# Kernel tuning notes

Hardware: AMD Instinct MI355X
Metric: run time of the kernel (lower is better)

The kernel has to match this reference:

```python
import jax, jax.numpy as jnp
import numpy as np

MUL = 128
LS = (0, 1, 2, 3, 4)
LMAX = 4
DIM = MUL * sum(2 * l + 1 for l in LS)   # 3200
NUM_IRREPS = MUL * len(LS)               # 640
NUM_M = [MUL * (LMAX + 1 - m) for m in range(LMAX + 1)]
N = 16384


def _expm(A, order=24, squarings=10):
    A = A / (2.0 ** squarings)
    E = np.eye(A.shape[0])
    T = np.eye(A.shape[0])
    for k in range(1, order):
        T = T @ A / k
        E = E + T
    for _ in range(squarings):
        E = E @ E
    return E


def _su2_generators(j):
    m = np.arange(-j, j)
    raising = np.diag(-np.sqrt(j * (j + 1) - m * (m + 1)), k=-1).astype(complex)
    m = np.arange(-j + 1, j + 1)
    lowering = np.diag(np.sqrt(j * (j + 1) - m * (m - 1)), k=1).astype(complex)
    m = np.arange(-j, j + 1)
    return np.stack([0.5 * (raising + lowering), np.diag(1j * m), -0.5j * (raising - lowering)])


def _q_real_to_complex(l):
    q = np.zeros((2 * l + 1, 2 * l + 1), dtype=complex)
    for m in range(-l, 0):
        q[l + m, l + abs(m)] = 1 / np.sqrt(2)
        q[l + m, l - abs(m)] = -1j / np.sqrt(2)
    q[l, l] = 1.0
    for m in range(1, l + 1):
        q[l + m, l + abs(m)] = (-1) ** m / np.sqrt(2)
        q[l + m, l - abs(m)] = 1j * (-1) ** m / np.sqrt(2)
    return (-1j) ** l * q


def _so3_generators(l):
    X = _su2_generators(l)
    Q = _q_real_to_complex(l)
    return np.real(np.conj(Q.T)[None] @ X @ Q[None])


def _J(l):
    # J_l = pi rotation about (x+y)/sqrt(2): conjugates z_rot (y-axis) into the beta (x-axis) rotation,
    # reproducing e3nn's _Jd used in wigner_D = Z(a) J Z(b) J Z(g).
    X = _so3_generators(l)
    return _expm(np.pi * (X[0] + X[1]) / np.sqrt(2.0))


JMAT = {l: jnp.asarray(_J(l), dtype=jnp.float32) for l in LS if l > 0}


def _build_mask():
    mask = np.zeros((LMAX + 1, DIM), dtype=bool)
    cur = 0
    for l in LS:
        for k in range(MUL):
            base = cur + k * (2 * l + 1)
            for m in range(l + 1):
                if m == 0:
                    mask[0, base + l] = True
                else:
                    mask[m, base + l + m] = True
                    mask[m, base + l - m] = True
        cur += MUL * (2 * l + 1)
    return mask


_MASK = _build_mask()
IDX = [np.nonzero(_MASK[m])[0] for m in range(LMAX + 1)]  # same layout for in and out irreps


def _z_rot(angle, l):
    d = 2 * l + 1
    freqs = jnp.arange(l, -l - 1, -1, dtype=angle.dtype)
    c = jnp.cos(freqs * angle[:, None])
    s = jnp.sin(freqs * angle[:, None])
    i = jnp.arange(d)
    M = jnp.zeros((angle.shape[0], d, d), angle.dtype)
    M = M.at[:, i, i].set(c)
    M = M.at[:, i, d - 1 - i].add(s)
    return M


def _wigner(l, alpha, beta, gamma):
    J = JMAT[l].astype(alpha.dtype)
    return _z_rot(alpha, l) @ J @ _z_rot(beta, l) @ J @ _z_rot(gamma, l)


def _forward(x, R, fc0_w, fc0_b, w_ms):
    n = x.shape[0]
    # xyz_to_angles(R[:, [1, 2, 0]])
    v = jnp.stack([R[:, 1], R[:, 2], R[:, 0]], axis=-1)
    v = v / jnp.clip(jnp.linalg.norm(v, axis=-1, keepdims=True), 1e-12)
    v = jnp.clip(v, -1.0, 1.0)
    beta = jnp.arccos(v[:, 1])
    alpha = jnp.arctan2(v[:, 0], v[:, 2])
    gamma = jnp.zeros_like(alpha)
    rots = {l: _wigner(l, alpha, beta, gamma) for l in LS if l > 0}
    # rotate input blocks; the l=0 block of x_rot stays zero (exactly as the torch source)
    parts = []
    off = 0
    for l in LS:
        d = 2 * l + 1
        size = MUL * d
        if l == 0:
            parts.append(jnp.zeros((n, size), x.dtype))
        else:
            blk = x[:, off:off + size].reshape(n, MUL, d)
            parts.append(jnp.einsum('nji,nmj->nmi', rots[l], blk).reshape(n, size))
        off += size
    x_rot = jnp.concatenate(parts, axis=1)
    out = jnp.zeros((n, DIM), x.dtype)
    # m = 0 path (radial_emb=False => w = ones, a no-op multiply)
    out = out.at[:, IDX[0]].add(x_rot[:, IDX[0]] @ fc0_w.T + fc0_b)
    # m >= 1 SO(2) paths
    for m in range(1, LMAX + 1):
        co = NUM_M[m]
        seg = x_rot[:, IDX[m]].reshape(n, 2, co)
        y = jnp.einsum('nct,ot->nco', seg, w_ms[m - 1])  # (n, 2, 2*co)
        re = y[:, 0, :co] - y[:, 1, co:]
        im = y[:, 0, co:] + y[:, 1, :co]
        out = out.at[:, IDX[m]].add(jnp.stack((re, im), axis=1).reshape(n, -1))
    # rotate output blocks (l=0 untouched)
    parts = []
    off = 0
    for l in LS:
        d = 2 * l + 1
        size = MUL * d
        blk = out[:, off:off + size]
        if l > 0:
            blk = jnp.einsum('nji,nmj->nmi', rots[l], blk.reshape(n, MUL, d)).reshape(n, size)
        parts.append(blk)
        off += size
    return jnp.concatenate(parts, axis=1)


def setup_inputs() -> dict:
    key = jax.random.key(0)
    ks = jax.random.split(key, 8)
    x = jax.random.normal(ks[0], (N, DIM), jnp.float32)
    R = jax.random.normal(ks[1], (N, 3), jnp.float32)
    fc0_w = jax.random.normal(ks[2], (NUM_IRREPS, NUM_IRREPS), jnp.float32) / np.float32(np.sqrt(NUM_IRREPS))
    fc0_b = jnp.zeros((NUM_IRREPS,), jnp.float32)
    w1 = jax.random.normal(ks[3], (2 * NUM_M[1], NUM_M[1]), jnp.float32) / np.float32(np.sqrt(2.0 * NUM_M[1]))
    w2 = jax.random.normal(ks[4], (2 * NUM_M[2], NUM_M[2]), jnp.float32) / np.float32(np.sqrt(2.0 * NUM_M[2]))
    w3 = jax.random.normal(ks[5], (2 * NUM_M[3], NUM_M[3]), jnp.float32) / np.float32(np.sqrt(2.0 * NUM_M[3]))
    w4 = jax.random.normal(ks[6], (2 * NUM_M[4], NUM_M[4]), jnp.float32) / np.float32(np.sqrt(2.0 * NUM_M[4]))
    return {"x": x, "R": R, "fc0_w": fc0_w, "fc0_b": fc0_b, "w1": w1, "w2": w2, "w3": w3, "w4": w4}


def reference(x, R, fc0_w, fc0_b, w1, w2, w3, w4):
    return _forward(x, R, fc0_w, fc0_b, (w1, w2, w3, w4))
```

## Files before the change

### kernel.cpp

```cpp
#include <hip/hip_runtime.h>
#include <hip/hip_bf16.h>
#include <math.h>

#define N_ROWS 16384
#define DIM    3200

using short8  = __attribute__((ext_vector_type(8))) short;
using floatx4 = __attribute__((ext_vector_type(4))) float;

__device__ const int c_K [5] = {640, 1024, 768, 512, 256};
__device__ const int c_UO[5] = {0, 640, 1664, 2432, 2944};
__device__ const int c_WO[5] = {0, 409600, 1458176, 2048000, 2310144};
__device__ const int c_mOf[25]  = {0,0,0,0,0, 1,1,1,1,1,1,1,1, 2,2,2,2,2,2, 3,3,3,3, 4,4};
__device__ const int c_ntOf[25] = {0,1,2,3,4, 0,1,2,3,4,5,6,7, 0,1,2,3,4,5, 0,1,2,3, 0,1};

__device__ __forceinline__ constexpr int joff_of(int l) { return l==1 ? 0 : l==2 ? 9 : l==3 ? 34 : 83; }
__device__ __forceinline__ constexpr int gO(int m)      { return m==1 ? 640 : m==2 ? 1664 : m==3 ? 2432 : 2944; }

__global__ __launch_bounds__(128) void build_J(float* __restrict__ Jout)
{
    const int l = blockIdx.x + 1;
    const int d = 2*l + 1;
    const int dd = d*d;
    const int tid = threadIdx.x;
    __shared__ double Qr[81], Qi[81], Xr[81], Xi[81];
    __shared__ double M1r[81], M1i[81];
    __shared__ double Am[81], Em[81], Tm[81], Tn[81];

    if (tid == 0) {
        for (int e = 0; e < dd; ++e) { Qr[e]=0; Qi[e]=0; Xr[e]=0; Xi[e]=0; }
        const double jj = (double)l;
        for (int i = 0; i < d-1; ++i) {
            double mm = -jj + (double)i;
            Xr[(i+1)*d + i] += 0.5 * (-sqrt(jj*(jj+1.0) - mm*(mm+1.0)));
            double m2 = -jj + 1.0 + (double)i;
            Xr[i*d + (i+1)] += 0.5 * ( sqrt(jj*(jj+1.0) - m2*(m2-1.0)));
        }
        for (int i = 0; i < d; ++i) Xi[i*d + i] = -jj + (double)i;
        const double is2 = 1.0 / sqrt(2.0);
        for (int mm = -l; mm < 0; ++mm) {
            int r = l + mm;
            Qr[r*d + (l - mm)] = is2;
            Qi[r*d + (l + mm)] = -is2;
        }
        Qr[l*d + l] = 1.0;
        for (int mm = 1; mm <= l; ++mm) {
            int r = l + mm;
            double sgn = (mm & 1) ? -1.0 : 1.0;
            Qr[r*d + (l + mm)] = sgn * is2;
            Qi[r*d + (l - mm)] = sgn * is2;
        }
        double fr, fi;
        switch (l & 3) {
            case 0: fr = 1;  fi = 0;  break;
            case 1: fr = 0;  fi = -1; break;
            case 2: fr = -1; fi = 0;  break;
            default: fr = 0; fi = 1;  break;
        }
        for (int e = 0; e < dd; ++e) {
            double qr = Qr[e], qi = Qi[e];
            Qr[e] = qr*fr - qi*fi;
            Qi[e] = qr*fi + qi*fr;
        }
    }
    __syncthreads();
    const int i = tid / d;
    const int j = tid % d;
    if (tid < dd) {
        double ar = 0, ai = 0;
        for (int k = 0; k < d; ++k) {
            double xr = Xr[i*d+k], xi = Xi[i*d+k];
            double qr = Qr[k*d+j], qi = Qi[k*d+j];
            ar += xr*qr - xi*qi;
            ai += xr*qi + xi*qr;
        }
        M1r[tid] = ar; M1i[tid] = ai;
    }
    __syncthreads();
    if (tid < dd) {
        double ar = 0;
        for (int k = 0; k < d; ++k)
            ar += Qr[k*d+i]*M1r[k*d+j] + Qi[k*d+i]*M1i[k*d+j];
        const double scale = 3.14159265358979323846 / sqrt(2.0) / 1024.0;
        Am[tid] = ar * scale;
        Em[tid] = (i == j) ? 1.0 : 0.0;
        Tm[tid] = (i == j) ? 1.0 : 0.0;
    }
    __syncthreads();
    for (int k = 1; k < 24; ++k) {
        if (tid < dd) {
            double s = 0;
            for (int b = 0; b < d; ++b) s += Tm[i*d+b] * Am[b*d+j];
            Tn[tid] = s / (double)k;
        }
        __syncthreads();
        if (tid < dd) { Tm[tid] = Tn[tid]; Em[tid] += Tn[tid]; }
        __syncthreads();
    }
    for (int s = 0; s < 10; ++s) {
        if (tid < dd) {
            double v = 0;
            for (int b = 0; b < d; ++b) v += Em[i*d+b] * Em[b*d+j];
            Tn[tid] = v;
        }
        __syncthreads();
        if (tid < dd) Em[tid] = Tn[tid];
        __syncthreads();
    }
    if (tid < dd) Jout[joff_of(l) + tid] = (float)Em[tid];
}

__global__ __launch_bounds__(256) void prep_w(
    const float* __restrict__ fc0_w,
    const float* __restrict__ w1, const float* __restrict__ w2,
    const float* __restrict__ w3, const float* __restrict__ w4,
    __hip_bfloat16* __restrict__ Wall)
{
    const int m = blockIdx.y;
    const int idx = blockIdx.x * 256 + threadIdx.x;
    if (m == 0) {
        if (idx < 640*640) Wall[idx] = __float2bfloat16(fc0_w[idx]);
        return;
    }
    const int co = 128 * (5 - m);
    const int C  = 2 * co;
    if (idx >= C*C) return;
    const float* wm = (m==1) ? w1 : (m==2) ? w2 : (m==3) ? w3 : w4;
    const int jj = idx / C;
    const int tt = idx - jj * C;
    float v;
    if (jj < co) {
        v = (tt < co) ? wm[jj*co + tt] : -wm[(co + jj)*co + (tt - co)];
    } else {
        v = (tt < co) ? wm[jj*co + tt] :  wm[(jj - co)*co + (tt - co)];
    }
    Wall[c_WO[m] + idx] = __float2bfloat16(v);
}

__global__ __launch_bounds__(256) void build_trig(
    const float* __restrict__ R, float* __restrict__ trig)
{
    const int row = blockIdx.x * 256 + threadIdx.x;
    if (row >= N_ROWS) return;
    float r0 = R[row*3+0], r1 = R[row*3+1], r2 = R[row*3+2];
    float nrm = sqrtf(r0*r0 + r1*r1 + r2*r2);
    nrm = fmaxf(nrm, 1e-12f);
    float vx = r1/nrm, vy = r2/nrm, vz = r0/nrm;
    vx = fminf(1.f, fmaxf(-1.f, vx));
    vy = fminf(1.f, fmaxf(-1.f, vy));
    vz = fminf(1.f, fmaxf(-1.f, vz));
    float beta  = acosf(vy);
    float alpha = atan2f(vx, vz);
    float* t = trig + row*20;
#pragma unroll
    for (int m = 0; m < 5; ++m) {
        float s, c;
        sincosf(alpha * (float)m, &s, &c);
        t[m] = c; t[5+m] = s;
        sincosf(beta * (float)m, &s, &c);
        t[10+m] = c; t[15+m] = s;
    }
}

__global__ __launch_bounds__(256) void build_D(
    const float* __restrict__ Jws, const float* __restrict__ trig,
    float* __restrict__ Dws)
{
    const int gid = blockIdx.x * 256 + threadIdx.x;
    if (gid >= N_ROWS * 164) return;
    const int row = gid / 164;
    const int e   = gid - row * 164;
    int l, base;
    if (e < 9)       { l = 1; base = 0;  }
    else if (e < 34) { l = 2; base = 9;  }
    else if (e < 83) { l = 3; base = 34; }
    else             { l = 4; base = 83; }
    const int d = 2*l + 1;
    const int loc = e - base;
    const int i = loc / d, j = loc - i*d;
    const float* Jp = Jws + base;
    const float* t  = trig + row*20;
    float pij = 0.f, pdj = 0.f;
    for (int b = 0; b < d; ++b) {
        int f = l - b; int af = f < 0 ? -f : f;
        float cb = t[10 + af];
        float sb = (b >= l) ? t[15 + b - l] : -t[15 + l - b];
        float zr  = Jp[i*d + b]*cb + Jp[i*d + (d-1-b)]*sb;
        float zr2 = Jp[(d-1-i)*d + b]*cb + Jp[(d-1-i)*d + (d-1-b)]*sb;
        float jb  = Jp[b*d + j];
        pij += zr  * jb;
        pdj += zr2 * jb;
    }
    int f = l - i; int af = f < 0 ? -f : f;
    float ca = t[af];
    float sa = (f > 0) ? t[5 + f] : ((f < 0) ? -t[5 + af] : 0.f);
    Dws[gid] = ca * pij + sa * pdj;
}

template<int L>
__device__ __forceinline__ void rot_one(const float* __restrict__ xr,
                                        const float* __restrict__ Dl,
                                        __hip_bfloat16* __restrict__ Urow, int k)
{
    constexpr int d = 2*L + 1;
    float xv[d], y[d];
    const float* xp = xr + 128*L*L + k*d;
#pragma unroll
    for (int j = 0; j < d; ++j) xv[j] = xp[j];
#pragma unroll
    for (int q = 0; q < d; ++q) {
        float acc = 0.f;
#pragma unroll
        for (int j = 0; j < d; ++j) acc += Dl[j*d + q] * xv[j];
        y[q] = acc;
    }
    Urow[L*128 + k] = __float2bfloat16(y[L]);
#pragma unroll
    for (int m = 1; m <= L; ++m) {
        unsigned short lo = __builtin_bit_cast(unsigned short, __float2bfloat16(y[L-m]));
        unsigned short hi = __builtin_bit_cast(unsigned short, __float2bfloat16(y[L+m]));
        unsigned int pack = ((unsigned int)hi << 16) | lo;
        *(unsigned int*)(Urow + gO(m) + 2*((L-m)*128 + k)) = pack;
    }
}

template<int L>
__device__ __forceinline__ void unrot_one(const __hip_bfloat16* __restrict__ Yrow,
                                          const float* __restrict__ Dl,
                                          float* __restrict__ orow, int k)
{
    constexpr int d = 2*L + 1;
    float yv[d];
    yv[L] = __bfloat162float(Yrow[L*128 + k]);
#pragma unroll
    for (int m = 1; m <= L; ++m) {
        unsigned int pack = *(const unsigned int*)(Yrow + gO(m) + 2*((L-m)*128 + k));
        unsigned short lo = (unsigned short)(pack & 0xffffu);
        unsigned short hi = (unsigned short)(pack >> 16);
        yv[L-m] = __bfloat162float(__builtin_bit_cast(__hip_bfloat16, lo));
        yv[L+m] = __bfloat162float(__builtin_bit_cast(__hip_bfloat16, hi));
    }
    float* op = orow + 128*L*L + k*d;
#pragma unroll
    for (int i = 0; i < d; ++i) {
        float acc = 0.f;
#pragma unroll
        for (int j = 0; j < d; ++j) acc += Dl[j*d + i] * yv[j];
        op[i] = acc;
    }
}

__global__ __launch_bounds__(256) void rot_gather(
    const float* __restrict__ x, const float* __restrict__ Dws,
    __hip_bfloat16* __restrict__ U)
{
    const int gid = blockIdx.x * 256 + threadIdx.x;
    const int row = gid / 640;
    const int c   = gid - row * 640;
    const int l = c >> 7, k = c & 127;
    const float* xr = x + (size_t)row * DIM;
    __hip_bfloat16* Urow = U + (size_t)row * DIM;
    const float* Dm = Dws + (size_t)row * 164;
    switch (l) {
        case 0: Urow[k] = __float2bfloat16(0.f); break;
        case 1: rot_one<1>(xr, Dm + 0,  Urow, k); break;
        case 2: rot_one<2>(xr, Dm + 9,  Urow, k); break;
        case 3: rot_one<3>(xr, Dm + 34, Urow, k); break;
        case 4: rot_one<4>(xr, Dm + 83, Urow, k); break;
    }
}

__device__ __forceinline__ void g2lds16(const void* g, void* l) {
    __builtin_amdgcn_global_load_lds(
        (const __attribute__((address_space(1))) void*)g,
        (__attribute__((address_space(3))) void*)l, 16, 0, 0);
}

__global__ __launch_bounds__(256) void gemm_bt(
    const __hip_bfloat16* __restrict__ U, const __hip_bfloat16* __restrict__ W,
    const float* __restrict__ bias, __hip_bfloat16* __restrict__ Y)
{
    const int by = blockIdx.y;
    const int m  = c_mOf[by];
    const int nt = c_ntOf[by];
    const int K  = c_K[m];
    const int row0 = blockIdx.x * 128;
    const __hip_bfloat16* Ablk = U + (size_t)row0*DIM + c_UO[m];
    const __hip_bfloat16* Bblk = W + c_WO[m] + (size_t)nt*128*K;
    __shared__ __align__(16) __hip_bfloat16 As[128*32];
    __shared__ __align__(16) __hip_bfloat16 Bs[128*32];
    const int tid  = threadIdx.x;
    const int lane = tid & 63, w = tid >> 6;
    const int frow = lane & 15, quad = lane >> 4;
    const int wm = (w >> 1)*64, wn = (w & 1)*64;

    floatx4 acc[4][4];
#pragma unroll
    for (int i = 0; i < 4; ++i)
#pragma unroll
        for (int j = 0; j < 4; ++j) acc[i][j] = (floatx4){0.f, 0.f, 0.f, 0.f};

    const int c1 = w*64 + lane;
    const int c2 = c1 + 256;
    for (int k0 = 0; k0 < K; k0 += 32) {
        g2lds16(Ablk + (size_t)(c1 >> 2)*DIM + k0 + (c1 & 3)*8, (char*)As + w*1024);
        g2lds16(Ablk + (size_t)(c2 >> 2)*DIM + k0 + (c2 & 3)*8, (char*)As + 4096 + w*1024);
        g2lds16(Bblk + (size_t)(c1 >> 2)*K   + k0 + (c1 & 3)*8, (char*)Bs + w*1024);
        g2lds16(Bblk + (size_t)(c2 >> 2)*K   + k0 + (c2 & 3)*8, (char*)Bs + 4096 + w*1024);
        __syncthreads();
        short8 a[4], b[4];
#pragma unroll
        for (int t = 0; t < 4; ++t) {
            a[t] = *(const short8*)((const char*)As + (((wm + t*16 + frow)*32 + quad*8) * 2));
            b[t] = *(const short8*)((const char*)Bs + (((wn + t*16 + frow)*32 + quad*8) * 2));
        }
#pragma unroll
        for (int i = 0; i < 4; ++i)
#pragma unroll
            for (int j = 0; j < 4; ++j)
                acc[i][j] = __builtin_amdgcn_mfma_f32_16x16x32_bf16(a[i], b[j], acc[i][j], 0, 0, 0);
        __syncthreads();
    }
#pragma unroll
    for (int i = 0; i < 4; ++i) {
        const int r0 = row0 + wm + i*16 + quad*4;
#pragma unroll
        for (int j = 0; j < 4; ++j) {
            const int n = wn + j*16 + frow;
            const float bv = (m == 0) ? bias[nt*128 + n] : 0.f;
            const size_t colg = (size_t)c_UO[m] + nt*128 + n;
#pragma unroll
            for (int r = 0; r < 4; ++r)
                Y[(size_t)(r0 + r)*DIM + colg] = __float2bfloat16(acc[i][j][r] + bv);
        }
    }
}

__global__ __launch_bounds__(256) void ungather_rot(
    const __hip_bfloat16* __restrict__ Y, const float* __restrict__ Dws,
    float* __restrict__ out)
{
    const int gid = blockIdx.x * 256 + threadIdx.x;
    const int row = gid / 640;
    const int c   = gid - row * 640;
    const int l = c >> 7, k = c & 127;
    const __hip_bfloat16* Yrow = Y + (size_t)row * DIM;
    float* orow = out + (size_t)row * DIM;
    const float* Dm = Dws + (size_t)row * 164;
    switch (l) {
        case 0: orow[k] = __bfloat162float(Yrow[k]); break;
        case 1: unrot_one<1>(Yrow, Dm + 0,  orow, k); break;
        case 2: unrot_one<2>(Yrow, Dm + 9,  orow, k); break;
        case 3: unrot_one<3>(Yrow, Dm + 34, orow, k); break;
        case 4: unrot_one<4>(Yrow, Dm + 83, orow, k); break;
    }
}

extern "C" void kernel_launch(void* const* d_in, const int* in_sizes, int n_in,
                              void* d_out, int out_size, void* d_ws, size_t ws_size,
                              hipStream_t stream)
{
    (void)in_sizes; (void)n_in; (void)out_size; (void)ws_size;
    const float* x     = (const float*)d_in[0];
    const float* R     = (const float*)d_in[1];
    const float* fc0_w = (const float*)d_in[2];
    const float* fc0_b = (const float*)d_in[3];
    const float* w1    = (const float*)d_in[4];
    const float* w2    = (const float*)d_in[5];
    const float* w3    = (const float*)d_in[6];
    const float* w4    = (const float*)d_in[7];
    float* out = (float*)d_out;

    char* ws = (char*)d_ws;
    float*          Jws  = (float*)ws;
    __hip_bfloat16* Wall = (__hip_bfloat16*)(ws + 1024);
    float*          Dws  = (float*)(ws + 4752384);
    __hip_bfloat16* U    = (__hip_bfloat16*)(ws + 15500288);
    __hip_bfloat16* Y    = (__hip_bfloat16*)(ws + 120357888);
    float*          trig = (float*)(ws + 120357888);

    build_J     <<<dim3(4),         dim3(128), 0, stream>>>(Jws);
    prep_w      <<<dim3(4096, 5),   dim3(256), 0, stream>>>(fc0_w, w1, w2, w3, w4, Wall);
    build_trig  <<<dim3(64),        dim3(256), 0, stream>>>(R, trig);
    build_D     <<<dim3(10496),     dim3(256), 0, stream>>>(Jws, trig, Dws);
    rot_gather  <<<dim3(40960),     dim3(256), 0, stream>>>(x, Dws, U);
    gemm_bt     <<<dim3(128, 25),   dim3(256), 0, stream>>>(U, Wall, fc0_b, Y);
    ungather_rot<<<dim3(40960),     dim3(256), 0, stream>>>(Y, Dws, out);
}
```

Before: 680.4 us.

## Rewrite block GEMM with 256x256 tiles, 4-stage LDS pipeline and swizzle

The block-diagonal bf16 GEMM now uses 512-thread workgroups computing 256x256 output tiles over a flat 832-block grid. A block-index remap groups neighbouring tiles for cache locality. K-slices stream into a 4-deep ring of XOR-swizzled LDS buffers via global_load_lds with explicit vmcnt waits, replacing the double __syncthreads per step, and the MFMA section runs at raised wave priority. The larger tiles raise operand reuse and hide load latency, but they need 128KB of LDS per block and overshoot the 640-wide m=0 block, so edge columns are masked.

After: 663.7 us. -2.5%, faster.

```diff
diff --git a/kernel.cpp b/kernel.cpp
--- a/kernel.cpp
+++ b/kernel.cpp
@@ -11,8 +11,8 @@
 __device__ const int c_K [5] = {640, 1024, 768, 512, 256};
 __device__ const int c_UO[5] = {0, 640, 1664, 2432, 2944};
 __device__ const int c_WO[5] = {0, 409600, 1458176, 2048000, 2310144};
-__device__ const int c_mOf[25]  = {0,0,0,0,0, 1,1,1,1,1,1,1,1, 2,2,2,2,2,2, 3,3,3,3, 4,4};
-__device__ const int c_ntOf[25] = {0,1,2,3,4, 0,1,2,3,4,5,6,7, 0,1,2,3,4,5, 0,1,2,3, 0,1};
+__device__ const int c_m13 [13] = {0,0,0, 1,1,1,1, 2,2,2, 3,3, 4};
+__device__ const int c_nt13[13] = {0,1,2, 0,1,2,3, 0,1,2, 0,1, 0};
 
 __device__ __forceinline__ constexpr int joff_of(int l) { return l==1 ? 0 : l==2 ? 9 : l==3 ? 34 : 83; }
 __device__ __forceinline__ constexpr int gO(int m)      { return m==1 ? 640 : m==2 ? 1664 : m==3 ? 2432 : 2944; }
@@ -276,62 +276,121 @@
         (__attribute__((address_space(3))) void*)l, 16, 0, 0);
 }
 
-__global__ __launch_bounds__(256) void gemm_bt(
+__device__ __forceinline__ int swz(int x) { return x ^ (((x >> 7) & 7) << 4); }
+
+__global__ __launch_bounds__(512, 2) void gemm_bt(
     const __hip_bfloat16* __restrict__ U, const __hip_bfloat16* __restrict__ W,
     const float* __restrict__ bias, __hip_bfloat16* __restrict__ Y)
 {
-    const int by = blockIdx.y;
-    const int m  = c_mOf[by];
-    const int nt = c_ntOf[by];
-    const int K  = c_K[m];
-    const int row0 = blockIdx.x * 128;
-    const __hip_bfloat16* Ablk = U + (size_t)row0*DIM + c_UO[m];
-    const __hip_bfloat16* Bblk = W + c_WO[m] + (size_t)nt*128*K;
-    __shared__ __align__(16) __hip_bfloat16 As[128*32];
-    __shared__ __align__(16) __hip_bfloat16 Bs[128*32];
+    const int bid = blockIdx.x;
+    const int wg  = (bid & 7) * 104 + (bid >> 3);
+    const int rt  = wg / 13;
+    const int ct  = wg - rt * 13;
+    const int m   = c_m13[ct];
+    const int nt2 = c_nt13[ct];
+    const int K   = c_K[m];
+    const int NT  = K >> 5;
+    const int row0 = rt * 256;
+
+    const __hip_bfloat16* Ablk = U + (size_t)row0 * DIM + c_UO[m];
+    const __hip_bfloat16* Bblk = W + c_WO[m] + (size_t)nt2 * 256 * K;
+
+    __shared__ __align__(16) char lds[131072];
+
     const int tid  = threadIdx.x;
     const int lane = tid & 63, w = tid >> 6;
     const int frow = lane & 15, quad = lane >> 4;
-    const int wm = (w >> 1)*64, wn = (w & 1)*64;
-
-    floatx4 acc[4][4];
-#pragma unroll
-    for (int i = 0; i < 4; ++i)
+    const int wmi  = w >> 2, wni = w & 3;
+
+    const __hip_bfloat16* srcA[2];
+    const __hip_bfloat16* srcB[2];
+#pragma unroll
+    for (int t = 0; t < 2; ++t) {
+        const int o   = tid * 16 + t * 8192;
+        const int lam = swz(o);
+        const int row = lam >> 7, colb = lam & 127;
+        const int idx = row + ((colb >> 6) & 1) * 128;
+        const int ke  = (colb & 63) >> 1;
+        srcA[t] = Ablk + (size_t)(idx) * DIM + ke;
+        srcB[t] = Bblk + (size_t)(idx) * K   + ke;
+    }
+
+    int aoff[8], boff[4];
+#pragma unroll
+    for (int i = 0; i < 8; ++i)
+        aoff[i] = swz((i*16 + frow) * 128 + wmi * 64 + quad * 16);
+#pragma unroll
+    for (int j = 0; j < 4; ++j)
+        boff[j] = swz(((wni & 1) * 64 + j*16 + frow) * 128 + (wni >> 1) * 64 + quad * 16);
+
+    floatx4 acc[8][4];
+#pragma unroll
+    for (int i = 0; i < 8; ++i)
 #pragma unroll
         for (int j = 0; j < 4; ++j) acc[i][j] = (floatx4){0.f, 0.f, 0.f, 0.f};
 
-    const int c1 = w*64 + lane;
-    const int c2 = c1 + 256;
-    for (int k0 = 0; k0 < K; k0 += 32) {
-        g2lds16(Ablk + (size_t)(c1 >> 2)*DIM + k0 + (c1 & 3)*8, (char*)As + w*1024);
-        g2lds16(Ablk + (size_t)(c2 >> 2)*DIM + k0 + (c2 & 3)*8, (char*)As + 4096 + w*1024);
-        g2lds16(Bblk + (size_t)(c1 >> 2)*K   + k0 + (c1 & 3)*8, (char*)Bs + w*1024);
-        g2lds16(Bblk + (size_t)(c2 >> 2)*K   + k0 + (c2 & 3)*8, (char*)Bs + 4096 + w*1024);
-        __syncthreads();
-        short8 a[4], b[4];
-#pragma unroll
-        for (int t = 0; t < 4; ++t) {
-            a[t] = *(const short8*)((const char*)As + (((wm + t*16 + frow)*32 + quad*8) * 2));
-            b[t] = *(const short8*)((const char*)Bs + (((wn + t*16 + frow)*32 + quad*8) * 2));
-        }
-#pragma unroll
-        for (int i = 0; i < 4; ++i)
+#pragma unroll
+    for (int p = 0; p < 3; ++p) {
+        char* Ad = lds + p * 16384;
+        char* Bd = lds + 65536 + p * 16384;
+        g2lds16(srcA[0] + p*32, Ad + w*1024);
+        g2lds16(srcA[1] + p*32, Ad + 8192 + w*1024);
+        g2lds16(srcB[0] + p*32, Bd + w*1024);
+        g2lds16(srcB[1] + p*32, Bd + 8192 + w*1024);
+    }
+    __builtin_amdgcn_sched_barrier(0);
+    asm volatile("s_waitcnt vmcnt(8)" ::: "memory");
+    __builtin_amdgcn_s_barrier();
+    __builtin_amdgcn_sched_barrier(0);
+
+    for (int kt = 0; kt < NT; ++kt) {
+        const char* Ab = lds + (kt & 3) * 16384;
+        const char* Bb = lds + 65536 + (kt & 3) * 16384;
+        short8 a[8], b[4];
+#pragma unroll
+        for (int i = 0; i < 8; ++i) a[i] = *(const short8*)(Ab + aoff[i]);
+#pragma unroll
+        for (int j = 0; j < 4; ++j) b[j] = *(const short8*)(Bb + boff[j]);
+
+        {
+            int ks = kt + 3; if (ks > NT - 1) ks = NT - 1;
+            char* Ad = lds + ((kt + 3) & 3) * 16384;
+            char* Bd = lds + 65536 + ((kt + 3) & 3) * 16384;
+            g2lds16(srcA[0] + ks*32, Ad + w*1024);
+            g2lds16(srcA[1] + ks*32, Ad + 8192 + w*1024);
+            g2lds16(srcB[0] + ks*32, Bd + w*1024);
+            g2lds16(srcB[1] + ks*32, Bd + 8192 + w*1024);
+        }
+        __builtin_amdgcn_sched_barrier(0);
+
+        __builtin_amdgcn_s_setprio(1);
+#pragma unroll
+        for (int i = 0; i < 8; ++i)
 #pragma unroll
             for (int j = 0; j < 4; ++j)
                 acc[i][j] = __builtin_amdgcn_mfma_f32_16x16x32_bf16(a[i], b[j], acc[i][j], 0, 0, 0);
-        __syncthreads();
-    }
-#pragma unroll
-    for (int i = 0; i < 4; ++i) {
-        const int r0 = row0 + wm + i*16 + quad*4;
+        __builtin_amdgcn_s_setprio(0);
+
+        __builtin_amdgcn_sched_barrier(0);
+        asm volatile("s_waitcnt vmcnt(8)" ::: "memory");
+        __builtin_amdgcn_s_barrier();
+        __builtin_amdgcn_sched_barrier(0);
+    }
+    asm volatile("s_waitcnt vmcnt(0)" ::: "memory");
+
+#pragma unroll
+    for (int i = 0; i < 8; ++i) {
+        const int grow = row0 + wmi*128 + i*16 + quad*4;
 #pragma unroll
         for (int j = 0; j < 4; ++j) {
-            const int n = wn + j*16 + frow;
-            const float bv = (m == 0) ? bias[nt*128 + n] : 0.f;
-            const size_t colg = (size_t)c_UO[m] + nt*128 + n;
-#pragma unroll
-            for (int r = 0; r < 4; ++r)
-                Y[(size_t)(r0 + r)*DIM + colg] = __float2bfloat16(acc[i][j][r] + bv);
+            const int col = nt2*256 + wni*64 + j*16 + frow;
+            if (col < K) {
+                const float bv = (m == 0) ? bias[col] : 0.f;
+                const size_t cg = (size_t)c_UO[m] + col;
+#pragma unroll
+                for (int r = 0; r < 4; ++r)
+                    Y[(size_t)(grow + r)*DIM + cg] = __float2bfloat16(acc[i][j][r] + bv);
+            }
         }
     }
 }
@@ -384,6 +443,6 @@
     build_trig  <<<dim3(64),        dim3(256), 0, stream>>>(R, trig);
     build_D     <<<dim3(10496),     dim3(256), 0, stream>>>(Jws, trig, Dws);
     rot_gather  <<<dim3(40960),     dim3(256), 0, stream>>>(x, Dws, U);
-    gemm_bt     <<<dim3(128, 25),   dim3(256), 0, stream>>>(U, Wall, fc0_b, Y);
+    gemm_bt     <<<dim3(832),       dim3(512), 0, stream>>>(U, Wall, fc0_b, Y);
     ungather_rot<<<dim3(40960),     dim3(256), 0, stream>>>(Y, Dws, out);
 }
```
